# Performance work log

Hardware: AMD Instinct MI355X
Metric: run time of the kernel (lower is better)

The kernel has to match this reference:

```python
import jax, jax.numpy as jnp
import numpy as np

B = 131072
N_X = 64
H = 512
LD = 8                      # latent_dim
N_THETA = 1 + LD + LD * (LD + 1) // 2   # 45
N_STEPS = 20
_IU = np.triu_indices(LD)   # static upper-tri index pairs for quadratic terms


def _layernorm(x, g, b, eps=1e-5):
    m = jnp.mean(x, axis=-1, keepdims=True)
    v = jnp.var(x, axis=-1, keepdims=True)
    return (x - m) * jax.lax.rsqrt(v + eps) * g + b


def _library(z):
    # Theta(z) = [1, z, upper-tri quadratic terms]  -> [B, N_THETA]
    ones = jnp.ones((z.shape[0], 1), z.dtype)
    quad = z[:, _IU[0]] * z[:, _IU[1]]
    return jnp.concatenate([ones, z, quad], axis=1)


def setup_inputs() -> dict:
    key = jax.random.key(0)
    ks = jax.random.split(key, 16)

    def W(k, fan_in, fan_out):
        # kaiming_normal (relu gain) as in the torch init
        return jax.random.normal(k, (fan_in, fan_out), jnp.float32) * np.sqrt(2.0 / fan_in)

    inp = {
        "x0_norm": jax.random.normal(ks[0], (B, N_X), jnp.float32),
        "log10_Dt_norm": jax.random.uniform(ks[1], (B, 1), jnp.float32),
        "Dt_mean": 0,
        "Dt_std": 1,
        # encoder: n_x -> 512 -> 512 -> latent (LN+SiLU between, final Tanh)
        "enc_W1": W(ks[2], N_X, H), "enc_b1": jnp.zeros((H,), jnp.float32),
        "enc_g1": jnp.ones((H,), jnp.float32), "enc_be1": jnp.zeros((H,), jnp.float32),
        "enc_W2": W(ks[3], H, H), "enc_b2": jnp.zeros((H,), jnp.float32),
        "enc_g2": jnp.ones((H,), jnp.float32), "enc_be2": jnp.zeros((H,), jnp.float32),
        "enc_W3": W(ks[4], H, LD), "enc_b3": jnp.zeros((LD,), jnp.float32),
        # decoder: latent -> 512 -> 512 -> n_x (LN+SiLU between, no final act)
        "dec_W1": W(ks[5], LD, H), "dec_b1": jnp.zeros((H,), jnp.float32),
        "dec_g1": jnp.ones((H,), jnp.float32), "dec_be1": jnp.zeros((H,), jnp.float32),
        "dec_W2": W(ks[6], H, H), "dec_b2": jnp.zeros((H,), jnp.float32),
        "dec_g2": jnp.ones((H,), jnp.float32), "dec_be2": jnp.zeros((H,), jnp.float32),
        "dec_W3": W(ks[7], H, N_X), "dec_b3": jnp.zeros((N_X,), jnp.float32),
        "Xi": 0.01 * jax.random.normal(ks[8], (N_THETA, LD), jnp.float32),
    }
    return inp


def reference(x0_norm, log10_Dt_norm, Dt_mean, Dt_std,
              enc_W1, enc_b1, enc_g1, enc_be1, enc_W2, enc_b2, enc_g2, enc_be2,
              enc_W3, enc_b3,
              dec_W1, dec_b1, dec_g1, dec_be1, dec_W2, dec_b2, dec_g2, dec_be2,
              dec_W3, dec_b3, Xi):
    # 1. encode: z0 = phi(x0)
    h = jax.nn.silu(_layernorm(x0_norm @ enc_W1 + enc_b1, enc_g1, enc_be1))
    h = jax.nn.silu(_layernorm(h @ enc_W2 + enc_b2, enc_g2, enc_be2))
    z0 = jnp.tanh(h @ enc_W3 + enc_b3)                       # [B, LD]

    # 2. Euler-integrate dz/dtau = Theta(z) Xi for N_STEPS fixed steps
    dt = log10_Dt_norm[:, :1] / N_STEPS                       # [B, 1]

    def step(z, _):
        zdot = _library(z) @ Xi                               # [B, LD]
        return z + zdot * dt, None

    z_t, _ = jax.lax.scan(step, z0, None, length=N_STEPS)

    # 3. decode: xhat = psi(z_t)
    h = jax.nn.silu(_layernorm(z_t @ dec_W1 + dec_b1, dec_g1, dec_be1))
    h = jax.nn.silu(_layernorm(h @ dec_W2 + dec_b2, dec_g2, dec_be2))
    xhat = h @ dec_W3 + dec_b3                                # [B, N_X]
    return xhat
```

## Files before the change

kernel.cpp:

```cpp
#include <hip/hip_runtime.h>
#include <hip/hip_bf16.h>
#include <math.h>

#define B_TOTAL 131072
#define NX 64
#define H 512
#define LD 8
#define NT 45
#define NSTEPS 20

#define NTH 512
#define BM 64
#define ASTR 520

#define OFF_EW1T 0
#define OFF_EW2T 32768
#define OFF_DW2T 294912
#define OFF_DW3T 557056
#define WS_ELEMS 589824
#define OFF_W3HI 589824
#define OFF_W3LO 598016
#define WS_ELEMS2 606208
#define ZT_OFF_BYTES (WS_ELEMS2 * 2)
#define WS_NEW_BYTES (ZT_OFF_BYTES + (size_t)B_TOTAL * LD * 4)

typedef __attribute__((ext_vector_type(8))) short short8;
typedef __attribute__((ext_vector_type(4))) float f32x4;

__device__ __forceinline__ ushort f2bf(float f) {
    union { float f; uint u; } v; v.f = f;
    uint u = v.u;
    u += 0x7fff + ((u >> 16) & 1);
    return (ushort)(u >> 16);
}
__device__ __forceinline__ float bf2f(ushort s) {
    union { uint u; float f; } v; v.u = ((uint)s) << 16;
    return v.f;
}
__device__ __forceinline__ float silu_f(float v) {
    return v / (1.0f + __expf(-v));
}

__global__ void prep_weights(const float* __restrict__ eW1, const float* __restrict__ eW2,
                             const float* __restrict__ dW2, const float* __restrict__ dW3,
                             const float* __restrict__ eW3, short* __restrict__ ws) {
    const int id = blockIdx.x * 256 + threadIdx.x;
    if (id < OFF_EW2T) {
        const int kc = id >> 14, n = (id >> 5) & 511, kk = id & 31;
        ws[id] = (short)f2bf(eW1[(kc * 32 + kk) * H + n]);
    } else if (id < OFF_DW2T) {
        const int j = id - OFF_EW2T;
        const int kc = j >> 14, n = (j >> 5) & 511, kk = j & 31;
        ws[id] = (short)f2bf(eW2[(kc * 32 + kk) * H + n]);
    } else if (id < OFF_DW3T) {
        const int j = id - OFF_DW2T;
        const int kc = j >> 14, n = (j >> 5) & 511, kk = j & 31;
        ws[id] = (short)f2bf(dW2[(kc * 32 + kk) * H + n]);
    } else if (id < WS_ELEMS) {
        const int j = id - OFF_DW3T;
        const int kc = j >> 11, n = (j >> 5) & 63, kk = j & 31;
        ws[id] = (short)f2bf(dW3[(kc * 32 + kk) * NX + n]);
    } else if (id < OFF_W3LO) {
        const int j = id - OFF_W3HI, n = j >> 9, k = j & 511;
        const float v = (n < LD) ? eW3[k * LD + n] : 0.f;
        ws[id] = (short)f2bf(v);
    } else if (id < WS_ELEMS2) {
        const int j = id - OFF_W3LO, n = j >> 9, k = j & 511;
        const float v = (n < LD) ? eW3[k * LD + n] : 0.f;
        const float hi = bf2f(f2bf(v));
        ws[id] = (short)f2bf(v - hi);
    }
}

template <int K, int N>
__device__ __forceinline__ void gemm_chunked(const short (*act)[ASTR], const short* __restrict__ WTc,
                                             f32x4 (&acc)[4][4], int w, int lm, int q) {
    constexpr int NC = K / 32;
    constexpr int CS = N * 32;
    const short* bp = WTc + (w * 64 + lm) * 32 + q * 8;
    short8 be[4], bo[4];
#pragma unroll
    for (int tt = 0; tt < 4; ++tt) be[tt] = *(const short8*)(bp + tt * 512);
#pragma unroll 1
    for (int kc = 0; kc < NC; kc += 2) {
        {
            const short* p = bp + (kc + 1) * CS;
#pragma unroll
            for (int tt = 0; tt < 4; ++tt) bo[tt] = *(const short8*)(p + tt * 512);
        }
        {
            const int k0 = kc * 32 + q * 8;
#pragma unroll
            for (int mt = 0; mt < 4; ++mt) {
                short8 a = *(const short8*)&act[mt * 16 + lm][k0];
#pragma unroll
                for (int tt = 0; tt < 4; ++tt)
                    acc[mt][tt] = __builtin_amdgcn_mfma_f32_16x16x32_bf16(a, be[tt], acc[mt][tt], 0, 0, 0);
            }
        }
        if (kc + 2 < NC) {
            const short* p = bp + (kc + 2) * CS;
#pragma unroll
            for (int tt = 0; tt < 4; ++tt) be[tt] = *(const short8*)(p + tt * 512);
        }
        {
            const int k0 = (kc + 1) * 32 + q * 8;
#pragma unroll
            for (int mt = 0; mt < 4; ++mt) {
                short8 a = *(const short8*)&act[mt * 16 + lm][k0];
#pragma unroll
                for (int tt = 0; tt < 4; ++tt)
                    acc[mt][tt] = __builtin_amdgcn_mfma_f32_16x16x32_bf16(a, bo[tt], acc[mt][tt], 0, 0, 0);
            }
        }
    }
}

__device__ __forceinline__ void ln_epi64(f32x4 (&acc)[4][4],
        const float* __restrict__ bias, const float* __restrict__ g, const float* __restrict__ be,
        short (*act)[ASTR], float (*p1)[8], float (*p2)[8], float (*rstat)[2],
        int w, int lane, int tid) {
    const int lm = lane & 15, q = lane >> 4;
    float cb[4], cg[4], cbe[4];
#pragma unroll
    for (int tt = 0; tt < 4; ++tt) {
        const int c = w * 64 + tt * 16 + lm;
        cb[tt] = bias[c]; cg[tt] = g[c]; cbe[tt] = be[c];
    }
#pragma unroll
    for (int mt = 0; mt < 4; ++mt) {
        float s1[4] = {0.f, 0.f, 0.f, 0.f}, s2[4] = {0.f, 0.f, 0.f, 0.f};
#pragma unroll
        for (int tt = 0; tt < 4; ++tt)
#pragma unroll
            for (int r = 0; r < 4; ++r) {
                float v = acc[mt][tt][r] + cb[tt];
                acc[mt][tt][r] = v;
                s1[r] += v;
                s2[r] += v * v;
            }
#pragma unroll
        for (int m = 1; m < 16; m <<= 1) {
#pragma unroll
            for (int r = 0; r < 4; ++r) {
                s1[r] += __shfl_xor(s1[r], m);
                s2[r] += __shfl_xor(s2[r], m);
            }
        }
        if (lm == 0) {
#pragma unroll
            for (int r = 0; r < 4; ++r) {
                const int row = mt * 16 + q * 4 + r;
                p1[row][w] = s1[r];
                p2[row][w] = s2[r];
            }
        }
    }
    __syncthreads();
    if (tid < BM) {
        float a = 0.f, b2 = 0.f;
#pragma unroll
        for (int j = 0; j < 8; ++j) { a += p1[tid][j]; b2 += p2[tid][j]; }
        const float mean = a * (1.0f / H);
        rstat[tid][0] = mean;
        rstat[tid][1] = rsqrtf(b2 * (1.0f / H) - mean * mean + 1e-5f);
    }
    __syncthreads();
#pragma unroll
    for (int mt = 0; mt < 4; ++mt) {
#pragma unroll
        for (int r = 0; r < 4; ++r) {
            const int row = mt * 16 + q * 4 + r;
            const float mu = rstat[row][0], rs = rstat[row][1];
#pragma unroll
            for (int tt = 0; tt < 4; ++tt) {
                const float v = (acc[mt][tt][r] - mu) * rs * cg[tt] + cbe[tt];
                act[row][w * 64 + tt * 16 + lm] = (short)f2bf(silu_f(v));
            }
        }
    }
    __syncthreads();
}

__global__ __launch_bounds__(NTH, 4) void sindy_enc_kernel(
        const float* __restrict__ x0, const float* __restrict__ logdt,
        const float* __restrict__ eb1, const float* __restrict__ eg1, const float* __restrict__ ebe1,
        const float* __restrict__ eb2, const float* __restrict__ eg2, const float* __restrict__ ebe2,
        const float* __restrict__ eb3, const float* __restrict__ Xi,
        const short* __restrict__ wsb, float* __restrict__ zt) {
    __shared__ __align__(16) short act[BM][ASTR];
    __shared__ __align__(16) float scratch[2048];
    __shared__ float rstat[BM][2];
    __shared__ float dtb[BM];
    __shared__ float xis[NT * LD];
    float (*p1)[8] = (float(*)[8])scratch;
    float (*p2)[8] = (float(*)[8])(scratch + 512);
    float (*partial)[BM][LD] = (float(*)[BM][LD])scratch;

    const int tid = threadIdx.x;
    const int w = tid >> 6, lane = tid & 63, lm = lane & 15, q = lane >> 4;
    const int row0 = blockIdx.x * BM;

    if (tid < NT * LD) xis[tid] = Xi[tid];
    if (tid < BM) dtb[tid] = logdt[row0 + tid] * (1.0f / NSTEPS);
    {
        const int r = tid >> 3, c8 = (tid & 7) * 8;
        const float* xr = &x0[(row0 + r) * NX + c8];
        const float4 va = *(const float4*)xr;
        const float4 vb = *(const float4*)(xr + 4);
        short8 sv;
        sv[0] = (short)f2bf(va.x); sv[1] = (short)f2bf(va.y);
        sv[2] = (short)f2bf(va.z); sv[3] = (short)f2bf(va.w);
        sv[4] = (short)f2bf(vb.x); sv[5] = (short)f2bf(vb.y);
        sv[6] = (short)f2bf(vb.z); sv[7] = (short)f2bf(vb.w);
        *(short8*)&act[r][c8] = sv;
    }
    __syncthreads();

    {
        f32x4 acc[4][4];
#pragma unroll
        for (int mt = 0; mt < 4; ++mt)
#pragma unroll
            for (int tt = 0; tt < 4; ++tt) acc[mt][tt] = (f32x4){0.f, 0.f, 0.f, 0.f};
        gemm_chunked<NX, H>(act, wsb + OFF_EW1T, acc, w, lm, q);
        ln_epi64(acc, eb1, eg1, ebe1, act, p1, p2, rstat, w, lane, tid);
    }

    {
        f32x4 acc[4][4];
#pragma unroll
        for (int mt = 0; mt < 4; ++mt)
#pragma unroll
            for (int tt = 0; tt < 4; ++tt) acc[mt][tt] = (f32x4){0.f, 0.f, 0.f, 0.f};
        gemm_chunked<H, H>(act, wsb + OFF_EW2T, acc, w, lm, q);
        ln_epi64(acc, eb2, eg2, ebe2, act, p1, p2, rstat, w, lane, tid);
    }

    float z0;
    {
        const short* W3H = wsb + OFF_W3HI;
        const short* W3L = wsb + OFF_W3LO;
        const int kq = w & 3, mh = w >> 2;
        f32x4 a3[2];
        a3[0] = (f32x4){0.f, 0.f, 0.f, 0.f};
        a3[1] = (f32x4){0.f, 0.f, 0.f, 0.f};
#pragma unroll
        for (int kc = 0; kc < 4; ++kc) {
            const int k0 = kq * 128 + kc * 32 + q * 8;
            short8 bh = *(const short8*)&W3H[lm * H + k0];
            short8 bl = *(const short8*)&W3L[lm * H + k0];
#pragma unroll
            for (int i = 0; i < 2; ++i) {
                short8 a = *(const short8*)&act[(mh * 2 + i) * 16 + lm][k0];
                a3[i] = __builtin_amdgcn_mfma_f32_16x16x32_bf16(a, bh, a3[i], 0, 0, 0);
                a3[i] = __builtin_amdgcn_mfma_f32_16x16x32_bf16(a, bl, a3[i], 0, 0, 0);
            }
        }
        if (lm < 8) {
#pragma unroll
            for (int i = 0; i < 2; ++i)
#pragma unroll
                for (int r = 0; r < 4; ++r)
                    partial[kq][(mh * 2 + i) * 16 + q * 4 + r][lm] = a3[i][r];
        }
        __syncthreads();
        {
            const int r = tid >> 3, c = tid & 7;
            const float s = partial[0][r][c] + partial[1][r][c] +
                            partial[2][r][c] + partial[3][r][c];
            z0 = tanhf(s + eb3[c]);
        }
    }

    {
        const int r = tid >> 3, c = tid & 7;
        const int lbase = lane & ~7;
        float xr[NT];
#pragma unroll
        for (int t = 0; t < NT; ++t) xr[t] = xis[t * LD + c];
        const float dtv = dtb[r];
        float zc = z0;
        for (int st = 0; st < NSTEPS; ++st) {
            float z[LD];
#pragma unroll
            for (int j = 0; j < LD; ++j) z[j] = __shfl(zc, lbase + j);
            float zd = xr[0];
#pragma unroll
            for (int j = 0; j < LD; ++j) zd += z[j] * xr[1 + j];
            int idx = 1 + LD;
#pragma unroll
            for (int i = 0; i < LD; ++i)
#pragma unroll
                for (int j = i; j < LD; ++j) {
                    zd += z[i] * z[j] * xr[idx];
                    ++idx;
                }
            zc += zd * dtv;
        }
        zt[row0 * LD + tid] = zc;
    }
}

__global__ __launch_bounds__(NTH, 4) void sindy_dec_kernel(
        const float* __restrict__ zt,
        const float* __restrict__ dW1, const float* __restrict__ db1,
        const float* __restrict__ dg1, const float* __restrict__ dbe1,
        const float* __restrict__ db2, const float* __restrict__ dg2, const float* __restrict__ dbe2,
        const float* __restrict__ db3,
        const short* __restrict__ wsb, float* __restrict__ out) {
    __shared__ __align__(16) short act[BM][ASTR];
    __shared__ float p1[BM][8], p2[BM][8], rstat[BM][2];
    __shared__ __align__(16) float zbuf[BM][LD];
    const int tid = threadIdx.x;
    const int w = tid >> 6, lane = tid & 63, lm = lane & 15, q = lane >> 4;
    const int row0 = blockIdx.x * BM;

    ((float*)zbuf)[tid] = zt[row0 * LD + tid];
    __syncthreads();

    {
        f32x4 acc[4][4];
#pragma unroll
        for (int tt = 0; tt < 4; ++tt) {
            const int c = w * 64 + tt * 16 + lm;
            float wk[LD];
#pragma unroll
            for (int k = 0; k < LD; ++k) wk[k] = dW1[k * H + c];
#pragma unroll
            for (int mt = 0; mt < 4; ++mt)
#pragma unroll
                for (int r = 0; r < 4; ++r) {
                    const int row = mt * 16 + q * 4 + r;
                    float s = 0.f;
#pragma unroll
                    for (int k = 0; k < LD; ++k) s += zbuf[row][k] * wk[k];
                    acc[mt][tt][r] = s;
                }
        }
        ln_epi64(acc, db1, dg1, dbe1, act, p1, p2, rstat, w, lane, tid);
    }

    {
        f32x4 acc[4][4];
#pragma unroll
        for (int mt = 0; mt < 4; ++mt)
#pragma unroll
            for (int tt = 0; tt < 4; ++tt) acc[mt][tt] = (f32x4){0.f, 0.f, 0.f, 0.f};
        gemm_chunked<H, H>(act, wsb + OFF_DW2T, acc, w, lm, q);
        ln_epi64(acc, db2, dg2, dbe2, act, p1, p2, rstat, w, lane, tid);
    }

    {
        const short* W3c = wsb + OFF_DW3T;
        const int nt = w & 3, mtb = (w >> 2) << 1;
        const short* bp = W3c + (nt * 16 + lm) * 32 + q * 8;
        f32x4 a2[2];
        a2[0] = (f32x4){0.f, 0.f, 0.f, 0.f};
        a2[1] = (f32x4){0.f, 0.f, 0.f, 0.f};
        short8 be = *(const short8*)bp;
#pragma unroll 1
        for (int kc = 0; kc < 16; kc += 2) {
            short8 bo = *(const short8*)(bp + (kc + 1) * 2048);
            {
                const int k0 = kc * 32 + q * 8;
#pragma unroll
                for (int i = 0; i < 2; ++i) {
                    short8 a = *(const short8*)&act[(mtb + i) * 16 + lm][k0];
                    a2[i] = __builtin_amdgcn_mfma_f32_16x16x32_bf16(a, be, a2[i], 0, 0, 0);
                }
            }
            if (kc + 2 < 16) be = *(const short8*)(bp + (kc + 2) * 2048);
            {
                const int k0 = (kc + 1) * 32 + q * 8;
#pragma unroll
                for (int i = 0; i < 2; ++i) {
                    short8 a = *(const short8*)&act[(mtb + i) * 16 + lm][k0];
                    a2[i] = __builtin_amdgcn_mfma_f32_16x16x32_bf16(a, bo, a2[i], 0, 0, 0);
                }
            }
        }
        const int c = nt * 16 + lm;
        const float bb = db3[c];
#pragma unroll
        for (int i = 0; i < 2; ++i)
#pragma unroll
            for (int r = 0; r < 4; ++r) {
                const int row = (mtb + i) * 16 + q * 4 + r;
                out[(row0 + row) * NX + c] = a2[i][r] + bb;
            }
    }
}

#define FB_R 16
#define FB_STRIDE 520
#define FB_NT 256

__device__ __forceinline__ void fb_ln_silu(float buf[FB_R][FB_STRIDE],
                                           const float* __restrict__ g,
                                           const float* __restrict__ be, int t) {
    const int r = t >> 4, lane = t & 15;
    float s1 = 0.f, s2 = 0.f;
#pragma unroll
    for (int j = 0; j < H / 16; ++j) {
        float v = buf[r][lane + 16 * j];
        s1 += v; s2 += v * v;
    }
#pragma unroll
    for (int m = 8; m >= 1; m >>= 1) {
        s1 += __shfl_xor(s1, m, 16);
        s2 += __shfl_xor(s2, m, 16);
    }
    const float mean = s1 * (1.0f / H);
    const float var = s2 * (1.0f / H) - mean * mean;
    const float rstd = rsqrtf(var + 1e-5f);
#pragma unroll
    for (int j = 0; j < H / 16; ++j) {
        const int c = lane + 16 * j;
        float v = buf[r][c];
        buf[r][c] = silu_f((v - mean) * rstd * g[c] + be[c]);
    }
}

template <int K>
__device__ __forceinline__ void fb_gemmK(const float in[FB_R][FB_STRIDE], float out[FB_R][FB_STRIDE],
                                         const float* __restrict__ W,
                                         const float* __restrict__ b, int t) {
    const int c0 = t, c1 = t + 256;
    float acc0[FB_R], acc1[FB_R];
#pragma unroll
    for (int r = 0; r < FB_R; ++r) { acc0[r] = 0.f; acc1[r] = 0.f; }
    for (int k = 0; k < K; k += 4) {
        const float w00 = W[(k + 0) * H + c0], w10 = W[(k + 0) * H + c1];
        const float w01 = W[(k + 1) * H + c0], w11 = W[(k + 1) * H + c1];
        const float w02 = W[(k + 2) * H + c0], w12 = W[(k + 2) * H + c1];
        const float w03 = W[(k + 3) * H + c0], w13 = W[(k + 3) * H + c1];
#pragma unroll
        for (int r = 0; r < FB_R; ++r) {
            const float4 h = *(const float4*)&in[r][k];
            acc0[r] += h.x * w00 + h.y * w01 + h.z * w02 + h.w * w03;
            acc1[r] += h.x * w10 + h.y * w11 + h.z * w12 + h.w * w13;
        }
    }
    const float b0 = b[c0], b1 = b[c1];
#pragma unroll
    for (int r = 0; r < FB_R; ++r) {
        out[r][c0] = acc0[r] + b0;
        out[r][c1] = acc1[r] + b1;
    }
}

__global__ __launch_bounds__(FB_NT, 2) void sindy_fallback_kernel(
    const float* __restrict__ x0, const float* __restrict__ logdt,
    const float* __restrict__ eW1, const float* __restrict__ eb1,
    const float* __restrict__ eg1, const float* __restrict__ ebe1,
    const float* __restrict__ eW2, const float* __restrict__ eb2,
    const float* __restrict__ eg2, const float* __restrict__ ebe2,
    const float* __restrict__ eW3, const float* __restrict__ eb3,
    const float* __restrict__ dW1, const float* __restrict__ db1,
    const float* __restrict__ dg1, const float* __restrict__ dbe1,
    const float* __restrict__ dW2, const float* __restrict__ db2,
    const float* __restrict__ dg2, const float* __restrict__ dbe2,
    const float* __restrict__ dW3, const float* __restrict__ db3,
    const float* __restrict__ Xi, float* __restrict__ out) {
    __shared__ float sA[FB_R][FB_STRIDE];
    __shared__ float sB[FB_R][FB_STRIDE];
    __shared__ float zbuf[FB_R][LD];
    __shared__ float dtb[FB_R];
    __shared__ float xis[NT * LD];

    const int t = threadIdx.x;
    const int row0 = blockIdx.x * FB_R;

    for (int i = t; i < NT * LD; i += FB_NT) xis[i] = Xi[i];
    if (t < FB_R) dtb[t] = logdt[row0 + t] * (1.0f / NSTEPS);
    {
        const int r = t >> 4, k4 = (t & 15) * 4;
        *(float4*)&sB[r][k4] = *(const float4*)&x0[(row0 + r) * NX + k4];
    }
    __syncthreads();
    fb_gemmK<NX>(sB, sA, eW1, eb1, t);
    __syncthreads();
    fb_ln_silu(sA, eg1, ebe1, t);
    __syncthreads();
    fb_gemmK<H>(sA, sB, eW2, eb2, t);
    __syncthreads();
    fb_ln_silu(sB, eg2, ebe2, t);
    __syncthreads();
    if (t < FB_R * LD) {
        const int r = t >> 3, c = t & 7;
        float acc = 0.f;
        for (int k = 0; k < H; k += 4) {
            const float4 h = *(const float4*)&sB[r][k];
            acc += h.x * eW3[(k + 0) * LD + c] + h.y * eW3[(k + 1) * LD + c] +
                   h.z * eW3[(k + 2) * LD + c] + h.w * eW3[(k + 3) * LD + c];
        }
        zbuf[r][c] = tanhf(acc + eb3[c]);
    }
    __syncthreads();
    for (int s = 0; s < NSTEPS; ++s) {
        float zn = 0.f;
        const int r = t >> 3, c = t & 7;
        if (t < FB_R * LD) {
            float z[LD];
#pragma unroll
            for (int j = 0; j < LD; ++j) z[j] = zbuf[r][j];
            float zd = xis[c];
#pragma unroll
            for (int j = 0; j < LD; ++j) zd += z[j] * xis[(1 + j) * LD + c];
            int idx = 1 + LD;
#pragma unroll
            for (int i = 0; i < LD; ++i)
#pragma unroll
                for (int j = i; j < LD; ++j) {
                    zd += z[i] * z[j] * xis[idx * LD + c];
                    ++idx;
                }
            zn = z[c] + zd * dtb[r];
        }
        __syncthreads();
        if (t < FB_R * LD) zbuf[r][c] = zn;
        __syncthreads();
    }
    {
        const int c0 = t, c1 = t + 256;
        float acc0[FB_R], acc1[FB_R];
#pragma unroll
        for (int r = 0; r < FB_R; ++r) { acc0[r] = 0.f; acc1[r] = 0.f; }
#pragma unroll
        for (int k = 0; k < LD; ++k) {
            const float w0 = dW1[k * H + c0], w1 = dW1[k * H + c1];
#pragma unroll
            for (int r = 0; r < FB_R; ++r) {
                const float zv = zbuf[r][k];
                acc0[r] += zv * w0;
                acc1[r] += zv * w1;
            }
        }
        const float b0 = db1[c0], b1v = db1[c1];
#pragma unroll
        for (int r = 0; r < FB_R; ++r) {
            sA[r][c0] = acc0[r] + b0;
            sA[r][c1] = acc1[r] + b1v;
        }
    }
    __syncthreads();
    fb_ln_silu(sA, dg1, dbe1, t);
    __syncthreads();
    fb_gemmK<H>(sA, sB, dW2, db2, t);
    __syncthreads();
    fb_ln_silu(sB, dg2, dbe2, t);
    __syncthreads();
    {
        const int c = t & 63;
        const int rb = t >> 6;
        float acc[4] = {0.f, 0.f, 0.f, 0.f};
        for (int k = 0; k < H; k += 4) {
            const float w0 = dW3[(k + 0) * NX + c];
            const float w1 = dW3[(k + 1) * NX + c];
            const float w2 = dW3[(k + 2) * NX + c];
            const float w3 = dW3[(k + 3) * NX + c];
#pragma unroll
            for (int i = 0; i < 4; ++i) {
                const int r = rb + 4 * i;
                const float4 h = *(const float4*)&sB[r][k];
                acc[i] += h.x * w0 + h.y * w1 + h.z * w2 + h.w * w3;
            }
        }
        const float bb = db3[c];
#pragma unroll
        for (int i = 0; i < 4; ++i) {
            const int r = rb + 4 * i;
            out[(row0 + r) * NX + c] = acc[i] + bb;
        }
    }
}

extern "C" void kernel_launch(void* const* d_in, const int* in_sizes, int n_in,
                              void* d_out, int out_size, void* d_ws, size_t ws_size,
                              hipStream_t stream) {
    const float* x0    = (const float*)d_in[0];
    const float* logdt = (const float*)d_in[1];
    const float* eW1  = (const float*)d_in[4];
    const float* eb1  = (const float*)d_in[5];
    const float* eg1  = (const float*)d_in[6];
    const float* ebe1 = (const float*)d_in[7];
    const float* eW2  = (const float*)d_in[8];
    const float* eb2  = (const float*)d_in[9];
    const float* eg2  = (const float*)d_in[10];
    const float* ebe2 = (const float*)d_in[11];
    const float* eW3  = (const float*)d_in[12];
    const float* eb3  = (const float*)d_in[13];
    const float* dW1  = (const float*)d_in[14];
    const float* db1  = (const float*)d_in[15];
    const float* dg1  = (const float*)d_in[16];
    const float* dbe1 = (const float*)d_in[17];
    const float* dW2  = (const float*)d_in[18];
    const float* db2  = (const float*)d_in[19];
    const float* dg2  = (const float*)d_in[20];
    const float* dbe2 = (const float*)d_in[21];
    const float* dW3  = (const float*)d_in[22];
    const float* db3  = (const float*)d_in[23];
    const float* Xi   = (const float*)d_in[24];
    float* out = (float*)d_out;

    if (ws_size >= WS_NEW_BYTES) {
        short* wsb = (short*)d_ws;
        float* zt = (float*)((char*)d_ws + ZT_OFF_BYTES);
        prep_weights<<<WS_ELEMS2 / 256, 256, 0, stream>>>(eW1, eW2, dW2, dW3, eW3, wsb);
        sindy_enc_kernel<<<B_TOTAL / BM, NTH, 0, stream>>>(
            x0, logdt, eb1, eg1, ebe1, eb2, eg2, ebe2, eb3, Xi, wsb, zt);
        sindy_dec_kernel<<<B_TOTAL / BM, NTH, 0, stream>>>(
            zt, dW1, db1, dg1, dbe1, db2, dg2, dbe2, db3, wsb, out);
    } else {
        sindy_fallback_kernel<<<B_TOTAL / FB_R, FB_NT, 0, stream>>>(
            x0, logdt, eW1, eb1, eg1, ebe1, eW2, eb2, eg2, ebe2, eW3, eb3,
            dW1, db1, dg1, dbe1, dW2, db2, dg2, dbe2, dW3, db3, Xi, out);
    }
}
```

Baseline: 540.2 us.

## Double row tile to 128 per block in encoder and decoder kernels

Raises the block row tile from 64 to 128 so each weight fragment loaded from global memory feeds twice as many MFMA row tiles. This halves weight traffic per row in the 512x512 GEMMs. The accumulator arrays double to 8x4 per wave, and launch bounds drop from 4 to 2 blocks per CU, which cuts occupancy and raises register pressure. The encoder's final projection, the Euler loop (now two rows per thread) and the decoder's output GEMM (now one row tile per wave over all 64 columns) are remapped to match.

```diff
diff --git a/kernel.cpp b/kernel.cpp
--- a/kernel.cpp
+++ b/kernel.cpp
@@ -10,7 +10,7 @@
 #define NSTEPS 20
 
 #define NTH 512
-#define BM 64
+#define BM 128
 #define ASTR 520
 
 #define OFF_EW1T 0
@@ -74,7 +74,7 @@
 
 template <int K, int N>
 __device__ __forceinline__ void gemm_chunked(const short (*act)[ASTR], const short* __restrict__ WTc,
-                                             f32x4 (&acc)[4][4], int w, int lm, int q) {
+                                             f32x4 (&acc)[8][4], int w, int lm, int q) {
     constexpr int NC = K / 32;
     constexpr int CS = N * 32;
     const short* bp = WTc + (w * 64 + lm) * 32 + q * 8;
@@ -91,7 +91,7 @@
         {
             const int k0 = kc * 32 + q * 8;
 #pragma unroll
-            for (int mt = 0; mt < 4; ++mt) {
+            for (int mt = 0; mt < 8; ++mt) {
                 short8 a = *(const short8*)&act[mt * 16 + lm][k0];
 #pragma unroll
                 for (int tt = 0; tt < 4; ++tt)
@@ -106,7 +106,7 @@
         {
             const int k0 = (kc + 1) * 32 + q * 8;
 #pragma unroll
-            for (int mt = 0; mt < 4; ++mt) {
+            for (int mt = 0; mt < 8; ++mt) {
                 short8 a = *(const short8*)&act[mt * 16 + lm][k0];
 #pragma unroll
                 for (int tt = 0; tt < 4; ++tt)
@@ -116,7 +116,7 @@
     }
 }
 
-__device__ __forceinline__ void ln_epi64(f32x4 (&acc)[4][4],
+__device__ __forceinline__ void ln_epi128(f32x4 (&acc)[8][4],
         const float* __restrict__ bias, const float* __restrict__ g, const float* __restrict__ be,
         short (*act)[ASTR], float (*p1)[8], float (*p2)[8], float (*rstat)[2],
         int w, int lane, int tid) {
@@ -128,7 +128,7 @@
         cb[tt] = bias[c]; cg[tt] = g[c]; cbe[tt] = be[c];
     }
 #pragma unroll
-    for (int mt = 0; mt < 4; ++mt) {
+    for (int mt = 0; mt < 8; ++mt) {
         float s1[4] = {0.f, 0.f, 0.f, 0.f}, s2[4] = {0.f, 0.f, 0.f, 0.f};
 #pragma unroll
         for (int tt = 0; tt < 4; ++tt)
@@ -167,7 +167,7 @@
     }
     __syncthreads();
 #pragma unroll
-    for (int mt = 0; mt < 4; ++mt) {
+    for (int mt = 0; mt < 8; ++mt) {
 #pragma unroll
         for (int r = 0; r < 4; ++r) {
             const int row = mt * 16 + q * 4 + r;
@@ -182,19 +182,19 @@
     __syncthreads();
 }
 
-__global__ __launch_bounds__(NTH, 4) void sindy_enc_kernel(
+__global__ __launch_bounds__(NTH, 2) void sindy_enc_kernel(
         const float* __restrict__ x0, const float* __restrict__ logdt,
         const float* __restrict__ eb1, const float* __restrict__ eg1, const float* __restrict__ ebe1,
         const float* __restrict__ eb2, const float* __restrict__ eg2, const float* __restrict__ ebe2,
         const float* __restrict__ eb3, const float* __restrict__ Xi,
         const short* __restrict__ wsb, float* __restrict__ zt) {
     __shared__ __align__(16) short act[BM][ASTR];
-    __shared__ __align__(16) float scratch[2048];
+    __shared__ __align__(16) float scratch[4096];
     __shared__ float rstat[BM][2];
     __shared__ float dtb[BM];
     __shared__ float xis[NT * LD];
     float (*p1)[8] = (float(*)[8])scratch;
-    float (*p2)[8] = (float(*)[8])(scratch + 512);
+    float (*p2)[8] = (float(*)[8])(scratch + 1024);
     float (*partial)[BM][LD] = (float(*)[BM][LD])scratch;
 
     const int tid = threadIdx.x;
@@ -204,73 +204,79 @@
     if (tid < NT * LD) xis[tid] = Xi[tid];
     if (tid < BM) dtb[tid] = logdt[row0 + tid] * (1.0f / NSTEPS);
     {
-        const int r = tid >> 3, c8 = (tid & 7) * 8;
-        const float* xr = &x0[(row0 + r) * NX + c8];
-        const float4 va = *(const float4*)xr;
-        const float4 vb = *(const float4*)(xr + 4);
-        short8 sv;
-        sv[0] = (short)f2bf(va.x); sv[1] = (short)f2bf(va.y);
-        sv[2] = (short)f2bf(va.z); sv[3] = (short)f2bf(va.w);
-        sv[4] = (short)f2bf(vb.x); sv[5] = (short)f2bf(vb.y);
-        sv[6] = (short)f2bf(vb.z); sv[7] = (short)f2bf(vb.w);
-        *(short8*)&act[r][c8] = sv;
-    }
-    __syncthreads();
-
-    {
-        f32x4 acc[4][4];
-#pragma unroll
-        for (int mt = 0; mt < 4; ++mt)
+        const int r = tid >> 2, c16 = (tid & 3) * 16;
+        const float* xr = &x0[(row0 + r) * NX + c16];
+#pragma unroll
+        for (int h = 0; h < 2; ++h) {
+            const float4 va = *(const float4*)(xr + h * 8);
+            const float4 vb = *(const float4*)(xr + h * 8 + 4);
+            short8 sv;
+            sv[0] = (short)f2bf(va.x); sv[1] = (short)f2bf(va.y);
+            sv[2] = (short)f2bf(va.z); sv[3] = (short)f2bf(va.w);
+            sv[4] = (short)f2bf(vb.x); sv[5] = (short)f2bf(vb.y);
+            sv[6] = (short)f2bf(vb.z); sv[7] = (short)f2bf(vb.w);
+            *(short8*)&act[r][c16 + h * 8] = sv;
+        }
+    }
+    __syncthreads();
+
+    {
+        f32x4 acc[8][4];
+#pragma unroll
+        for (int mt = 0; mt < 8; ++mt)
 #pragma unroll
             for (int tt = 0; tt < 4; ++tt) acc[mt][tt] = (f32x4){0.f, 0.f, 0.f, 0.f};
         gemm_chunked<NX, H>(act, wsb + OFF_EW1T, acc, w, lm, q);
-        ln_epi64(acc, eb1, eg1, ebe1, act, p1, p2, rstat, w, lane, tid);
-    }
-
-    {
-        f32x4 acc[4][4];
-#pragma unroll
-        for (int mt = 0; mt < 4; ++mt)
+        ln_epi128(acc, eb1, eg1, ebe1, act, p1, p2, rstat, w, lane, tid);
+    }
+
+    {
+        f32x4 acc[8][4];
+#pragma unroll
+        for (int mt = 0; mt < 8; ++mt)
 #pragma unroll
             for (int tt = 0; tt < 4; ++tt) acc[mt][tt] = (f32x4){0.f, 0.f, 0.f, 0.f};
         gemm_chunked<H, H>(act, wsb + OFF_EW2T, acc, w, lm, q);
-        ln_epi64(acc, eb2, eg2, ebe2, act, p1, p2, rstat, w, lane, tid);
-    }
-
-    float z0;
+        ln_epi128(acc, eb2, eg2, ebe2, act, p1, p2, rstat, w, lane, tid);
+    }
+
+    float zr0, zr1;
     {
         const short* W3H = wsb + OFF_W3HI;
         const short* W3L = wsb + OFF_W3LO;
         const int kq = w & 3, mh = w >> 2;
-        f32x4 a3[2];
-        a3[0] = (f32x4){0.f, 0.f, 0.f, 0.f};
-        a3[1] = (f32x4){0.f, 0.f, 0.f, 0.f};
+        f32x4 a3[4];
+#pragma unroll
+        for (int i = 0; i < 4; ++i) a3[i] = (f32x4){0.f, 0.f, 0.f, 0.f};
 #pragma unroll
         for (int kc = 0; kc < 4; ++kc) {
             const int k0 = kq * 128 + kc * 32 + q * 8;
             short8 bh = *(const short8*)&W3H[lm * H + k0];
             short8 bl = *(const short8*)&W3L[lm * H + k0];
 #pragma unroll
-            for (int i = 0; i < 2; ++i) {
-                short8 a = *(const short8*)&act[(mh * 2 + i) * 16 + lm][k0];
+            for (int i = 0; i < 4; ++i) {
+                short8 a = *(const short8*)&act[mh * 64 + i * 16 + lm][k0];
                 a3[i] = __builtin_amdgcn_mfma_f32_16x16x32_bf16(a, bh, a3[i], 0, 0, 0);
                 a3[i] = __builtin_amdgcn_mfma_f32_16x16x32_bf16(a, bl, a3[i], 0, 0, 0);
             }
         }
         if (lm < 8) {
 #pragma unroll
-            for (int i = 0; i < 2; ++i)
+            for (int i = 0; i < 4; ++i)
 #pragma unroll
                 for (int r = 0; r < 4; ++r)
-                    partial[kq][(mh * 2 + i) * 16 + q * 4 + r][lm] = a3[i][r];
+                    partial[kq][mh * 64 + i * 16 + q * 4 + r][lm] = a3[i][r];
         }
         __syncthreads();
-        {
-            const int r = tid >> 3, c = tid & 7;
-            const float s = partial[0][r][c] + partial[1][r][c] +
-                            partial[2][r][c] + partial[3][r][c];
-            z0 = tanhf(s + eb3[c]);
-        }
+        const int r = tid >> 3, c = tid & 7;
+        float s0 = 0.f, sB = 0.f;
+#pragma unroll
+        for (int k2 = 0; k2 < 4; ++k2) {
+            s0 += partial[k2][r][c];
+            sB += partial[k2][r + 64][c];
+        }
+        zr0 = tanhf(s0 + eb3[c]);
+        zr1 = tanhf(sB + eb3[c]);
     }
 
     {
@@ -279,30 +285,39 @@
         float xr[NT];
 #pragma unroll
         for (int t = 0; t < NT; ++t) xr[t] = xis[t * LD + c];
-        const float dtv = dtb[r];
-        float zc = z0;
+        const float dt0 = dtb[r], dt1 = dtb[r + 64];
+        float zc0 = zr0, zc1 = zr1;
         for (int st = 0; st < NSTEPS; ++st) {
-            float z[LD];
-#pragma unroll
-            for (int j = 0; j < LD; ++j) z[j] = __shfl(zc, lbase + j);
-            float zd = xr[0];
-#pragma unroll
-            for (int j = 0; j < LD; ++j) zd += z[j] * xr[1 + j];
+            float z0[LD], z1[LD];
+#pragma unroll
+            for (int j = 0; j < LD; ++j) {
+                z0[j] = __shfl(zc0, lbase + j);
+                z1[j] = __shfl(zc1, lbase + j);
+            }
+            float zd0 = xr[0], zd1 = xr[0];
+#pragma unroll
+            for (int j = 0; j < LD; ++j) {
+                zd0 += z0[j] * xr[1 + j];
+                zd1 += z1[j] * xr[1 + j];
+            }
             int idx = 1 + LD;
 #pragma unroll
             for (int i = 0; i < LD; ++i)
 #pragma unroll
                 for (int j = i; j < LD; ++j) {
-                    zd += z[i] * z[j] * xr[idx];
+                    zd0 += z0[i] * z0[j] * xr[idx];
+                    zd1 += z1[i] * z1[j] * xr[idx];
                     ++idx;
                 }
-            zc += zd * dtv;
-        }
-        zt[row0 * LD + tid] = zc;
-    }
-}
-
-__global__ __launch_bounds__(NTH, 4) void sindy_dec_kernel(
+            zc0 += zd0 * dt0;
+            zc1 += zd1 * dt1;
+        }
+        zt[row0 * LD + tid] = zc0;
+        zt[row0 * LD + 512 + tid] = zc1;
+    }
+}
+
+__global__ __launch_bounds__(NTH, 2) void sindy_dec_kernel(
         const float* __restrict__ zt,
         const float* __restrict__ dW1, const float* __restrict__ db1,
         const float* __restrict__ dg1, const float* __restrict__ dbe1,
@@ -317,10 +332,11 @@
     const int row0 = blockIdx.x * BM;
 
     ((float*)zbuf)[tid] = zt[row0 * LD + tid];
-    __syncthreads();
-
-    {
-        f32x4 acc[4][4];
+    ((float*)zbuf)[tid + 512] = zt[row0 * LD + 512 + tid];
+    __syncthreads();
+
+    {
+        f32x4 acc[8][4];
 #pragma unroll
         for (int tt = 0; tt < 4; ++tt) {
             const int c = w * 64 + tt * 16 + lm;
@@ -328,7 +344,7 @@
 #pragma unroll
             for (int k = 0; k < LD; ++k) wk[k] = dW1[k * H + c];
 #pragma unroll
-            for (int mt = 0; mt < 4; ++mt)
+            for (int mt = 0; mt < 8; ++mt)
 #pragma unroll
                 for (int r = 0; r < 4; ++r) {
                     const int row = mt * 16 + q * 4 + r;
@@ -338,57 +354,65 @@
                     acc[mt][tt][r] = s;
                 }
         }
-        ln_epi64(acc, db1, dg1, dbe1, act, p1, p2, rstat, w, lane, tid);
-    }
-
-    {
-        f32x4 acc[4][4];
-#pragma unroll
-        for (int mt = 0; mt < 4; ++mt)
+        ln_epi128(acc, db1, dg1, dbe1, act, p1, p2, rstat, w, lane, tid);
+    }
+
+    {
+        f32x4 acc[8][4];
+#pragma unroll
+        for (int mt = 0; mt < 8; ++mt)
 #pragma unroll
             for (int tt = 0; tt < 4; ++tt) acc[mt][tt] = (f32x4){0.f, 0.f, 0.f, 0.f};
         gemm_chunked<H, H>(act, wsb + OFF_DW2T, acc, w, lm, q);
-        ln_epi64(acc, db2, dg2, dbe2, act, p1, p2, rstat, w, lane, tid);
+        ln_epi128(acc, db2, dg2, dbe2, act, p1, p2, rstat, w, lane, tid);
     }
 
     {
         const short* W3c = wsb + OFF_DW3T;
-        const int nt = w & 3, mtb = (w >> 2) << 1;
-        const short* bp = W3c + (nt * 16 + lm) * 32 + q * 8;
-        f32x4 a2[2];
-        a2[0] = (f32x4){0.f, 0.f, 0.f, 0.f};
-        a2[1] = (f32x4){0.f, 0.f, 0.f, 0.f};
-        short8 be = *(const short8*)bp;
+        const short* bp = W3c + lm * 32 + q * 8;
+        f32x4 a4[4];
+#pragma unroll
+        for (int u = 0; u < 4; ++u) a4[u] = (f32x4){0.f, 0.f, 0.f, 0.f};
+        short8 be[4], bo[4];
+#pragma unroll
+        for (int u = 0; u < 4; ++u) be[u] = *(const short8*)(bp + u * 512);
 #pragma unroll 1
         for (int kc = 0; kc < 16; kc += 2) {
-            short8 bo = *(const short8*)(bp + (kc + 1) * 2048);
+            {
+                const short* p = bp + (kc + 1) * 2048;
+#pragma unroll
+                for (int u = 0; u < 4; ++u) bo[u] = *(const short8*)(p + u * 512);
+            }
             {
                 const int k0 = kc * 32 + q * 8;
-#pragma unroll
-                for (int i = 0; i < 2; ++i) {
-                    short8 a = *(const short8*)&act[(mtb + i) * 16 + lm][k0];
-                    a2[i] = __builtin_amdgcn_mfma_f32_16x16x32_bf16(a, be, a2[i], 0, 0, 0);
-                }
-            }
-            if (kc + 2 < 16) be = *(const short8*)(bp + (kc + 2) * 2048);
+                short8 a = *(const short8*)&act[w * 16 + lm][k0];
+#pragma unroll
+                for (int u = 0; u < 4; ++u)
+                    a4[u] = __builtin_amdgcn_mfma_f32_16x16x32_bf16(a, be[u], a4[u], 0, 0, 0);
+            }
+            if (kc + 2 < 16) {
+                const short* p = bp + (kc + 2) * 2048;
+#pragma unroll
+                for (int u = 0; u < 4; ++u) be[u] = *(const short8*)(p + u * 512);
+            }
             {
                 const int k0 = (kc + 1) * 32 + q * 8;
-#pragma unroll
-                for (int i = 0; i < 2; ++i) {
-                    short8 a = *(const short8*)&act[(mtb + i) * 16 + lm][k0];
-                    a2[i] = __builtin_amdgcn_mfma_f32_16x16x32_bf16(a, bo, a2[i], 0, 0, 0);
-                }
-            }
-        }
-        const int c = nt * 16 + lm;
-        const float bb = db3[c];
-#pragma unroll
-        for (int i = 0; i < 2; ++i)
+                short8 a = *(const short8*)&act[w * 16 + lm][k0];
+#pragma unroll
+                for (int u = 0; u < 4; ++u)
+                    a4[u] = __builtin_amdgcn_mfma_f32_16x16x32_bf16(a, bo[u], a4[u], 0, 0, 0);
+            }
+        }
+#pragma unroll
+        for (int u = 0; u < 4; ++u) {
+            const int c = u * 16 + lm;
+            const float bb = db3[c];
 #pragma unroll
             for (int r = 0; r < 4; ++r) {
-                const int row = (mtb + i) * 16 + q * 4 + r;
-                out[(row0 + row) * NX + c] = a2[i][r] + bb;
-            }
+                const int row = w * 16 + q * 4 + r;
+                out[(row0 + row) * NX + c] = a4[u][r] + bb;
+            }
+        }
     }
 }
 
```

Result: slower. 745.5 us (+38.0%).

## Run decoder first layer on MFMA with split-bf16 and simplify B-operand prefetch

Applied to the files above, without the earlier changes.

The decoder's K=8 first layer moves from scalar FP32 FMAs to a single MFMA per tile. The weights are pre-split into bf16 hi/lo parts in the workspace, and z is split the same way across the K lanes, which keeps near-fp32 accuracy. The double-buffered B prefetch in the chunked GEMMs and the decoder's last layer is replaced with a simple one-chunk-at-a-time load loop. The SINDy step now reads the quadratic Xi coefficients from LDS instead of keeping them in 36 registers, which cuts register pressure but adds LDS reads inside the Euler loop.

```diff
diff --git a/kernel.cpp b/kernel.cpp
--- a/kernel.cpp
+++ b/kernel.cpp
@@ -21,7 +21,9 @@
 #define OFF_W3HI 589824
 #define OFF_W3LO 598016
 #define WS_ELEMS2 606208
-#define ZT_OFF_BYTES (WS_ELEMS2 * 2)
+#define OFF_DW1P 606208
+#define WS_ELEMS3 622592
+#define ZT_OFF_BYTES (WS_ELEMS3 * 2)
 #define WS_NEW_BYTES (ZT_OFF_BYTES + (size_t)B_TOTAL * LD * 4)
 
 typedef __attribute__((ext_vector_type(8))) short short8;
@@ -43,7 +45,8 @@
 
 __global__ void prep_weights(const float* __restrict__ eW1, const float* __restrict__ eW2,
                              const float* __restrict__ dW2, const float* __restrict__ dW3,
-                             const float* __restrict__ eW3, short* __restrict__ ws) {
+                             const float* __restrict__ eW3, const float* __restrict__ dW1,
+                             short* __restrict__ ws) {
     const int id = blockIdx.x * 256 + threadIdx.x;
     if (id < OFF_EW2T) {
         const int kc = id >> 14, n = (id >> 5) & 511, kk = id & 31;
@@ -69,6 +72,13 @@
         const float v = (n < LD) ? eW3[k * LD + n] : 0.f;
         const float hi = bf2f(f2bf(v));
         ws[id] = (short)f2bf(v - hi);
+    } else if (id < WS_ELEMS3) {
+        const int j = id - OFF_DW1P;
+        const int n = j >> 5, s = j & 31;
+        const int k = s & 7;
+        const float v = dW1[k * H + n];
+        const ushort hi = f2bf(v);
+        ws[id] = (((s >> 3) & 1) == 0) ? (short)hi : (short)f2bf(v - bf2f(hi));
     }
 }
 
@@ -78,40 +88,19 @@
     constexpr int NC = K / 32;
     constexpr int CS = N * 32;
     const short* bp = WTc + (w * 64 + lm) * 32 + q * 8;
-    short8 be[4], bo[4];
-#pragma unroll
-    for (int tt = 0; tt < 4; ++tt) be[tt] = *(const short8*)(bp + tt * 512);
 #pragma unroll 1
-    for (int kc = 0; kc < NC; kc += 2) {
-        {
-            const short* p = bp + (kc + 1) * CS;
-#pragma unroll
-            for (int tt = 0; tt < 4; ++tt) bo[tt] = *(const short8*)(p + tt * 512);
-        }
-        {
-            const int k0 = kc * 32 + q * 8;
-#pragma unroll
-            for (int mt = 0; mt < 4; ++mt) {
-                short8 a = *(const short8*)&act[mt * 16 + lm][k0];
-#pragma unroll
-                for (int tt = 0; tt < 4; ++tt)
-                    acc[mt][tt] = __builtin_amdgcn_mfma_f32_16x16x32_bf16(a, be[tt], acc[mt][tt], 0, 0, 0);
-            }
-        }
-        if (kc + 2 < NC) {
-            const short* p = bp + (kc + 2) * CS;
-#pragma unroll
-            for (int tt = 0; tt < 4; ++tt) be[tt] = *(const short8*)(p + tt * 512);
-        }
-        {
-            const int k0 = (kc + 1) * 32 + q * 8;
-#pragma unroll
-            for (int mt = 0; mt < 4; ++mt) {
-                short8 a = *(const short8*)&act[mt * 16 + lm][k0];
-#pragma unroll
-                for (int tt = 0; tt < 4; ++tt)
-                    acc[mt][tt] = __builtin_amdgcn_mfma_f32_16x16x32_bf16(a, bo[tt], acc[mt][tt], 0, 0, 0);
-            }
+    for (int kc = 0; kc < NC; ++kc) {
+        short8 b[4];
+        const short* p = bp + kc * CS;
+#pragma unroll
+        for (int tt = 0; tt < 4; ++tt) b[tt] = *(const short8*)(p + tt * 512);
+        const int k0 = kc * 32 + q * 8;
+#pragma unroll
+        for (int mt = 0; mt < 4; ++mt) {
+            short8 a = *(const short8*)&act[mt * 16 + lm][k0];
+#pragma unroll
+            for (int tt = 0; tt < 4; ++tt)
+                acc[mt][tt] = __builtin_amdgcn_mfma_f32_16x16x32_bf16(a, b[tt], acc[mt][tt], 0, 0, 0);
         }
     }
 }
@@ -276,24 +265,24 @@
     {
         const int r = tid >> 3, c = tid & 7;
         const int lbase = lane & ~7;
-        float xr[NT];
-#pragma unroll
-        for (int t = 0; t < NT; ++t) xr[t] = xis[t * LD + c];
+        float xrl[1 + LD];
+#pragma unroll
+        for (int t = 0; t <= LD; ++t) xrl[t] = xis[t * LD + c];
         const float dtv = dtb[r];
         float zc = z0;
         for (int st = 0; st < NSTEPS; ++st) {
             float z[LD];
 #pragma unroll
             for (int j = 0; j < LD; ++j) z[j] = __shfl(zc, lbase + j);
-            float zd = xr[0];
-#pragma unroll
-            for (int j = 0; j < LD; ++j) zd += z[j] * xr[1 + j];
+            float zd = xrl[0];
+#pragma unroll
+            for (int j = 0; j < LD; ++j) zd += z[j] * xrl[1 + j];
             int idx = 1 + LD;
 #pragma unroll
             for (int i = 0; i < LD; ++i)
 #pragma unroll
                 for (int j = i; j < LD; ++j) {
-                    zd += z[i] * z[j] * xr[idx];
+                    zd += z[i] * z[j] * xis[idx * LD + c];
                     ++idx;
                 }
             zc += zd * dtv;
@@ -304,7 +293,7 @@
 
 __global__ __launch_bounds__(NTH, 4) void sindy_dec_kernel(
         const float* __restrict__ zt,
-        const float* __restrict__ dW1, const float* __restrict__ db1,
+        const float* __restrict__ db1,
         const float* __restrict__ dg1, const float* __restrict__ dbe1,
         const float* __restrict__ db2, const float* __restrict__ dg2, const float* __restrict__ dbe2,
         const float* __restrict__ db3,
@@ -320,23 +309,27 @@
     __syncthreads();
 
     {
+        const short* bp = wsb + OFF_DW1P + (w * 64 + lm) * 32 + q * 8;
+        short8 b[4];
+#pragma unroll
+        for (int tt = 0; tt < 4; ++tt) b[tt] = *(const short8*)(bp + tt * 512);
         f32x4 acc[4][4];
 #pragma unroll
-        for (int tt = 0; tt < 4; ++tt) {
-            const int c = w * 64 + tt * 16 + lm;
-            float wk[LD];
-#pragma unroll
-            for (int k = 0; k < LD; ++k) wk[k] = dW1[k * H + c];
-#pragma unroll
-            for (int mt = 0; mt < 4; ++mt)
-#pragma unroll
-                for (int r = 0; r < 4; ++r) {
-                    const int row = mt * 16 + q * 4 + r;
-                    float s = 0.f;
-#pragma unroll
-                    for (int k = 0; k < LD; ++k) s += zbuf[row][k] * wk[k];
-                    acc[mt][tt][r] = s;
-                }
+        for (int mt = 0; mt < 4; ++mt) {
+            const int row = mt * 16 + lm;
+            const float4 za = *(const float4*)&zbuf[row][0];
+            const float4 zb = *(const float4*)&zbuf[row][4];
+            float zv[LD] = {za.x, za.y, za.z, za.w, zb.x, zb.y, zb.z, zb.w};
+            short8 a;
+#pragma unroll
+            for (int j = 0; j < LD; ++j) {
+                const ushort h = f2bf(zv[j]);
+                a[j] = (q < 2) ? (short)h : (short)f2bf(zv[j] - bf2f(h));
+            }
+#pragma unroll
+            for (int tt = 0; tt < 4; ++tt)
+                acc[mt][tt] = __builtin_amdgcn_mfma_f32_16x16x32_bf16(
+                    a, b[tt], (f32x4){0.f, 0.f, 0.f, 0.f}, 0, 0, 0);
         }
         ln_epi64(acc, db1, dg1, dbe1, act, p1, p2, rstat, w, lane, tid);
     }
@@ -358,26 +351,14 @@
         f32x4 a2[2];
         a2[0] = (f32x4){0.f, 0.f, 0.f, 0.f};
         a2[1] = (f32x4){0.f, 0.f, 0.f, 0.f};
-        short8 be = *(const short8*)bp;
 #pragma unroll 1
-        for (int kc = 0; kc < 16; kc += 2) {
-            short8 bo = *(const short8*)(bp + (kc + 1) * 2048);
-            {
-                const int k0 = kc * 32 + q * 8;
-#pragma unroll
-                for (int i = 0; i < 2; ++i) {
-                    short8 a = *(const short8*)&act[(mtb + i) * 16 + lm][k0];
-                    a2[i] = __builtin_amdgcn_mfma_f32_16x16x32_bf16(a, be, a2[i], 0, 0, 0);
-                }
-            }
-            if (kc + 2 < 16) be = *(const short8*)(bp + (kc + 2) * 2048);
-            {
-                const int k0 = (kc + 1) * 32 + q * 8;
-#pragma unroll
-                for (int i = 0; i < 2; ++i) {
-                    short8 a = *(const short8*)&act[(mtb + i) * 16 + lm][k0];
-                    a2[i] = __builtin_amdgcn_mfma_f32_16x16x32_bf16(a, bo, a2[i], 0, 0, 0);
-                }
+        for (int kc = 0; kc < 16; ++kc) {
+            short8 b = *(const short8*)(bp + kc * 2048);
+            const int k0 = kc * 32 + q * 8;
+#pragma unroll
+            for (int i = 0; i < 2; ++i) {
+                short8 a = *(const short8*)&act[(mtb + i) * 16 + lm][k0];
+                a2[i] = __builtin_amdgcn_mfma_f32_16x16x32_bf16(a, b, a2[i], 0, 0, 0);
             }
         }
         const int c = nt * 16 + lm;
@@ -607,11 +588,11 @@
     if (ws_size >= WS_NEW_BYTES) {
         short* wsb = (short*)d_ws;
         float* zt = (float*)((char*)d_ws + ZT_OFF_BYTES);
-        prep_weights<<<WS_ELEMS2 / 256, 256, 0, stream>>>(eW1, eW2, dW2, dW3, eW3, wsb);
+        prep_weights<<<WS_ELEMS3 / 256, 256, 0, stream>>>(eW1, eW2, dW2, dW3, eW3, dW1, wsb);
         sindy_enc_kernel<<<B_TOTAL / BM, NTH, 0, stream>>>(
             x0, logdt, eb1, eg1, ebe1, eb2, eg2, ebe2, eb3, Xi, wsb, zt);
         sindy_dec_kernel<<<B_TOTAL / BM, NTH, 0, stream>>>(
-            zt, dW1, db1, dg1, dbe1, db2, dg2, dbe2, db3, wsb, out);
+            zt, db1, dg1, dbe1, db2, dg2, dbe2, db3, wsb, out);
     } else {
         sindy_fallback_kernel<<<B_TOTAL / FB_R, FB_NT, 0, stream>>>(
             x0, logdt, eW1, eb1, eg1, ebe1, eW2, eb2, eg2, ebe2, eW3, eb3,
```

New measurement: 469.4 us. 13.1% less time.
